# Kernel optimization log

Hardware: AMD Instinct MI355X
Metric: run time of the kernel (lower is better)

Reference implementation:

```python
import jax, jax.numpy as jnp
import numpy as np

DIM = 256
NUM_EXPERTS = 16
EXPERT_HIDDEN = 128
ROUTER_HIDDEN = 64
N_TOKENS = 32768


def setup_inputs() -> dict:
    key = jax.random.key(0)
    ks = jax.random.split(key, 9)
    s = lambda fan_in: 1.0 / np.sqrt(fan_in)
    x = jax.random.normal(ks[0], (N_TOKENS, DIM), dtype=jnp.float32)
    # Router params (Linear(DIM,64) -> ReLU -> Linear(64,E))
    r_w1 = jax.random.uniform(ks[1], (DIM, ROUTER_HIDDEN), jnp.float32, -s(DIM), s(DIM))
    r_b1 = jax.random.uniform(ks[2], (ROUTER_HIDDEN,), jnp.float32, -s(DIM), s(DIM))
    r_w2 = jax.random.uniform(ks[3], (ROUTER_HIDDEN, NUM_EXPERTS), jnp.float32, -s(ROUTER_HIDDEN), s(ROUTER_HIDDEN))
    r_b2 = jax.random.uniform(ks[4], (NUM_EXPERTS,), jnp.float32, -s(ROUTER_HIDDEN), s(ROUTER_HIDDEN))
    # Expert params, stacked over experts: Linear(DIM,128) -> Tanh -> Linear(128,DIM)
    e_w1 = jax.random.uniform(ks[5], (NUM_EXPERTS, DIM, EXPERT_HIDDEN), jnp.float32, -s(DIM), s(DIM))
    e_b1 = jax.random.uniform(ks[6], (NUM_EXPERTS, EXPERT_HIDDEN), jnp.float32, -s(DIM), s(DIM))
    e_w2 = jax.random.uniform(ks[7], (NUM_EXPERTS, EXPERT_HIDDEN, DIM), jnp.float32, -s(EXPERT_HIDDEN), s(EXPERT_HIDDEN))
    e_b2 = jax.random.uniform(ks[8], (NUM_EXPERTS, DIM), jnp.float32, -s(EXPERT_HIDDEN), s(EXPERT_HIDDEN))
    return {"x": x, "r_w1": r_w1, "r_b1": r_b1, "r_w2": r_w2, "r_b2": r_b2,
            "e_w1": e_w1, "e_b1": e_b1, "e_w2": e_w2, "e_b2": e_b2}


def reference(x, r_w1, r_b1, r_w2, r_b2, e_w1, e_b1, e_w2, e_b2):
    # Router: softmax(Linear(ReLU(Linear(x)))), temp=1.0
    h_r = jax.nn.relu(x @ r_w1 + r_b1)                      # [N, 64]
    w = jax.nn.softmax(h_r @ r_w2 + r_b2, axis=-1)          # [N, E]
    # All experts densely (faithful to the reference loop), batched over E.
    h = jnp.tanh(jnp.einsum('nd,edh->neh', x, e_w1) + e_b1[None, :, :])   # [N, E, H]
    outs = jnp.einsum('neh,ehd->ned', h, e_w2) + e_b2[None, :, :]         # [N, E, D]
    # Top-2 gating: mask, renormalize, combine.
    top_val, top_idx = jax.lax.top_k(w, 2)                  # [N, 2]
    n = w.shape[0]
    mask = jnp.zeros_like(w).at[jnp.arange(n)[:, None], top_idx].set(1.0)
    w_top = w * mask
    w_top = w_top / (jnp.sum(w_top, axis=-1, keepdims=True) + 1e-8)
    y_pred = jnp.einsum('ne,ned->nd', w_top, outs)          # [N, D]
    return (y_pred, w)
```

## Files before the change

kernel.cpp:

```cpp
#include <hip/hip_runtime.h>
#include <math.h>

#define NT 32768
#define DIM 256
#define NE 16
#define EH 128
#define RH 64
#define TB 64
#define NPERS 512

#define IB (NT * DIM)
#define WS_COUNTS (IB)
#define WS_OFFSETS (IB + 16)
#define WS_CURSORS (IB + 33)
#define WS_NBLK (IB + 49)
#define WS_TABLE (IB + 64)
#define WS_TOKE (IB + 4096)
#define WS_LIST (WS_TOKE + 2 * NT)
#define WS_TOKG (WS_LIST + 2 * NT)
#define WS_LIST_G (WS_TOKG + 2 * NT)
#define WS_END_I (WS_LIST_G + 2 * NT)
#define U_W1T (2 * WS_END_I)
#define U_W2T (U_W1T + NE * DIM * EH)
#define U_XG (U_W2T + NE * DIM * EH)

typedef __attribute__((ext_vector_type(4))) float f32x4;
typedef __attribute__((ext_vector_type(8))) short bf16x8;
typedef __attribute__((ext_vector_type(8))) unsigned short us8;

#define SWZ9(b) ((b) ^ (((b) >> 5) & 0x70))
#define SWZ8(b) ((b) ^ (((b) >> 4) & 0x70))

__device__ inline unsigned short f2bf(float f) {
    unsigned int bits = __builtin_bit_cast(unsigned int, f);
    bits += 0x7fffu + ((bits >> 16) & 1u);
    return (unsigned short)(bits >> 16);
}

__device__ inline float fast_tanh(float v) {
    float cv = fminf(fmaxf(v, -15.f), 15.f);
    float ex = __expf(2.f * cv);
    return (ex - 1.f) / (ex + 1.f);
}

__global__ __launch_bounds__(256) void router_kernel(
    const float* __restrict__ x,
    const float* __restrict__ rw1, const float* __restrict__ rb1,
    const float* __restrict__ rw2, const float* __restrict__ rb2,
    float* __restrict__ w_out, int* __restrict__ wsi, float* __restrict__ wsf)
{
    __shared__ float xT[64][68];
    __shared__ float w1s[64][64];
    __shared__ float hs[64][68];
    __shared__ float ls[64][20];
    __shared__ int scnt[16];

    const int tid = threadIdx.x;
    const int tok0 = blockIdx.x * 64;
    if (tid < 16) scnt[tid] = 0;

    float acc[4][4];
#pragma unroll
    for (int i = 0; i < 4; ++i)
#pragma unroll
        for (int j = 0; j < 4; ++j) acc[i][j] = 0.f;

    const int tt = (tid & 15) * 4;
    const int hh = (tid >> 4) * 4;

    for (int kc = 0; kc < 4; ++kc) {
        __syncthreads();
#pragma unroll
        for (int i = 0; i < 4; ++i) {
            int idx = tid + 256 * i;
            int t = idx >> 4;
            int d4 = (idx & 15) * 4;
            float4 v = *(const float4*)(x + (size_t)(tok0 + t) * DIM + kc * 64 + d4);
            xT[d4 + 0][t] = v.x; xT[d4 + 1][t] = v.y;
            xT[d4 + 2][t] = v.z; xT[d4 + 3][t] = v.w;
        }
#pragma unroll
        for (int i = 0; i < 4; ++i) {
            int idx = tid + 256 * i;
            int d = idx >> 4;
            int h4 = (idx & 15) * 4;
            *(float4*)&w1s[d][h4] = *(const float4*)(rw1 + (size_t)(kc * 64 + d) * RH + h4);
        }
        __syncthreads();
#pragma unroll 8
        for (int d = 0; d < 64; ++d) {
            const float4 xa4 = *(const float4*)&xT[d][tt];
            const float4 wv4 = *(const float4*)&w1s[d][hh];
            const float xa[4] = {xa4.x, xa4.y, xa4.z, xa4.w};
            const float wv[4] = {wv4.x, wv4.y, wv4.z, wv4.w};
#pragma unroll
            for (int i = 0; i < 4; ++i)
#pragma unroll
                for (int j = 0; j < 4; ++j)
                    acc[i][j] = fmaf(xa[i], wv[j], acc[i][j]);
        }
    }
    __syncthreads();
    {
        const float4 b4 = *(const float4*)(rb1 + hh);
        const float b[4] = {b4.x, b4.y, b4.z, b4.w};
#pragma unroll
        for (int i = 0; i < 4; ++i) {
            float4 hv;
            hv.x = fmaxf(acc[i][0] + b[0], 0.f);
            hv.y = fmaxf(acc[i][1] + b[1], 0.f);
            hv.z = fmaxf(acc[i][2] + b[2], 0.f);
            hv.w = fmaxf(acc[i][3] + b[3], 0.f);
            *(float4*)&hs[tt + i][hh] = hv;
        }
    }
    __syncthreads();
    {
        int tok = tid >> 2;
        int e0 = (tid & 3) * 4;
        float l[4] = {0.f, 0.f, 0.f, 0.f};
#pragma unroll 8
        for (int k = 0; k < 64; ++k) {
            float hv = hs[tok][k];
            float4 wv = *(const float4*)(rw2 + k * NE + e0);
            l[0] = fmaf(hv, wv.x, l[0]);
            l[1] = fmaf(hv, wv.y, l[1]);
            l[2] = fmaf(hv, wv.z, l[2]);
            l[3] = fmaf(hv, wv.w, l[3]);
        }
        float4 lb = *(const float4*)(rb2 + e0);
        ls[tok][e0 + 0] = l[0] + lb.x;
        ls[tok][e0 + 1] = l[1] + lb.y;
        ls[tok][e0 + 2] = l[2] + lb.z;
        ls[tok][e0 + 3] = l[3] + lb.w;
    }
    __syncthreads();
    if (tid < 64) {
        const int tok = tid;
        const int gt = tok0 + tok;
        float v[16];
        float m = -1e30f;
#pragma unroll
        for (int e = 0; e < 16; ++e) { v[e] = ls[tok][e]; m = fmaxf(m, v[e]); }
        float s = 0.f;
#pragma unroll
        for (int e = 0; e < 16; ++e) { v[e] = expf(v[e] - m); s += v[e]; }
        const float inv = 1.0f / s;
#pragma unroll
        for (int e = 0; e < 16; ++e) v[e] *= inv;
#pragma unroll
        for (int e = 0; e < 16; e += 4) {
            float4 wv = make_float4(v[e], v[e + 1], v[e + 2], v[e + 3]);
            *(float4*)(w_out + (size_t)gt * NE + e) = wv;
        }
        float v1 = -1.f, v2 = -1.f; int i1 = 0, i2 = 0;
#pragma unroll
        for (int e = 0; e < 16; ++e) {
            if (v[e] > v1) { v2 = v1; i2 = i1; v1 = v[e]; i1 = e; }
            else if (v[e] > v2) { v2 = v[e]; i2 = e; }
        }
        const float den = v1 + v2 + 1e-8f;
        atomicAdd(&scnt[i1], 1);
        atomicAdd(&scnt[i2], 1);
        wsi[WS_TOKE + 2 * gt + 0] = i1;
        wsi[WS_TOKE + 2 * gt + 1] = i2;
        wsf[WS_TOKG + 2 * gt + 0] = v1 / den;
        wsf[WS_TOKG + 2 * gt + 1] = v2 / den;
    }
    __syncthreads();
    if (tid < 16 && scnt[tid]) atomicAdd(&wsi[WS_COUNTS + tid], scnt[tid]);
}

__global__ __launch_bounds__(256) void wprep_kernel(
    const float* __restrict__ ew1, const float* __restrict__ ew2,
    unsigned short* __restrict__ w1t, unsigned short* __restrict__ w2t)
{
    __shared__ float t[64][65];
    int b = blockIdx.x;
    const float* src; unsigned short* dst; int R, C, tr, tc;
    if (b < 128) {
        int e = b >> 3, t8 = b & 7; tr = t8 >> 1; tc = t8 & 1;
        src = ew1 + (size_t)e * DIM * EH; R = DIM; C = EH;
        dst = w1t + (size_t)e * DIM * EH;
    } else {
        int b2 = b - 128; int e = b2 >> 3, t8 = b2 & 7; tr = t8 & 1; tc = t8 >> 1;
        src = ew2 + (size_t)e * EH * DIM; R = EH; C = DIM;
        dst = w2t + (size_t)e * EH * DIM;
    }
    const int R0 = tr * 64, C0 = tc * 64;
    const int tid = threadIdx.x;
#pragma unroll
    for (int q = 0; q < 4; ++q) {
        int r = (tid >> 4) + q * 16, c = (tid & 15) * 4;
        float4 v = *(const float4*)(src + (size_t)(R0 + r) * C + C0 + c);
        t[r][c] = v.x; t[r][c + 1] = v.y; t[r][c + 2] = v.z; t[r][c + 3] = v.w;
    }
    __syncthreads();
#pragma unroll
    for (int q = 0; q < 2; ++q) {
        int rp = (tid >> 3) + q * 32, c0 = (tid & 7) * 8;
        us8 u;
#pragma unroll
        for (int k = 0; k < 8; ++k) u[k] = f2bf(t[c0 + k][rp]);
        *(us8*)(dst + (size_t)(C0 + rp) * R + R0 + c0) = u;
    }
}

__global__ __launch_bounds__(64) void scan_kernel(int* __restrict__ wsi)
{
    __shared__ int soff[17], snc[16];
    const int tid = threadIdx.x;
    if (tid == 0) {
        int off = 0, nb = 0;
        soff[0] = 0;
        for (int e = 0; e < NE; ++e) {
            int c = wsi[WS_COUNTS + e];
            wsi[WS_CURSORS + e] = off;
            wsi[WS_OFFSETS + e] = off;
            off += c;
            soff[e + 1] = off;
            snc[e] = nb;
            nb += (c + TB - 1) / TB;
        }
        wsi[WS_OFFSETS + NE] = off;
        wsi[WS_NBLK] = nb;
    }
    __syncthreads();
    for (int e = 0; e < NE; ++e) {
        int nc = (soff[e + 1] - soff[e] + TB - 1) / TB;
        for (int k = tid; k < nc; k += 64)
            wsi[WS_TABLE + snc[e] + k] = (e << 16) | k;
    }
}

__global__ __launch_bounds__(256) void scatter_kernel(int* __restrict__ wsi, float* __restrict__ wsf)
{
    __shared__ int scnt[16], sbase[16];
    const int tid = threadIdx.x;
    const int t = blockIdx.x * 256 + tid;
    if (tid < 16) scnt[tid] = 0;
    __syncthreads();
    const int e0 = wsi[WS_TOKE + 2 * t + 0];
    const int e1 = wsi[WS_TOKE + 2 * t + 1];
    const int l0 = atomicAdd(&scnt[e0], 1);
    const int l1 = atomicAdd(&scnt[e1], 1);
    __syncthreads();
    if (tid < 16) sbase[tid] = scnt[tid] ? atomicAdd(&wsi[WS_CURSORS + tid], scnt[tid]) : 0;
    __syncthreads();
    const int p0 = sbase[e0] + l0;
    const int p1 = sbase[e1] + l1;
    wsi[WS_LIST + p0] = (t << 1);
    wsf[WS_LIST_G + p0] = wsf[WS_TOKG + 2 * t + 0];
    wsi[WS_LIST + p1] = (t << 1) | 1;
    wsf[WS_LIST_G + p1] = wsf[WS_TOKG + 2 * t + 1];
}

__global__ __launch_bounds__(256) void gather_kernel(
    const float* __restrict__ x, const int* __restrict__ wsi,
    unsigned short* __restrict__ xg)
{
    const int tid = threadIdx.x;
    const int p = blockIdx.x * 32 + (tid >> 3);
    const int sub = tid & 7;
    const int tok = wsi[WS_LIST + p] >> 1;
    const float* src = x + (size_t)tok * DIM + sub * 32;
    unsigned short* dst = xg + (size_t)p * DIM + sub * 32;
    float4 v[8];
#pragma unroll
    for (int i = 0; i < 8; ++i) v[i] = *(const float4*)(src + i * 4);
#pragma unroll
    for (int i = 0; i < 4; ++i) {
        us8 u;
        u[0] = f2bf(v[2 * i].x);     u[1] = f2bf(v[2 * i].y);
        u[2] = f2bf(v[2 * i].z);     u[3] = f2bf(v[2 * i].w);
        u[4] = f2bf(v[2 * i + 1].x); u[5] = f2bf(v[2 * i + 1].y);
        u[6] = f2bf(v[2 * i + 1].z); u[7] = f2bf(v[2 * i + 1].w);
        *(us8*)(dst + i * 8) = u;
    }
}

__global__ __launch_bounds__(256, 2) void expert_kernel(
    const unsigned short* __restrict__ xg,
    const float* __restrict__ eb1, const float* __restrict__ eb2,
    const unsigned short* __restrict__ w1t, const unsigned short* __restrict__ w2t,
    const int* __restrict__ wsi, const float* __restrict__ wsf,
    float* __restrict__ y, float* __restrict__ part1)
{
    __shared__ unsigned short smem[16384];
    __shared__ int sl[64];
    __shared__ float sg[64];

    const int nblk = wsi[WS_NBLK];
    const int tid = threadIdx.x;
    const int lane = tid & 63, w = tid >> 6;
    const int l15 = lane & 15;
    const int kq = lane >> 4;
    const int q4 = kq * 4;
    char* lds = (char*)smem;
    f32x4 zero4; zero4[0] = zero4[1] = zero4[2] = zero4[3] = 0.f;

    for (int bi = blockIdx.x; bi < nblk; bi += NPERS) {
        const int ent = wsi[WS_TABLE + bi];
        const int e = ent >> 16;
        const int c = ent & 0xffff;
        const int start = wsi[WS_OFFSETS + e] + c * TB;
        const int cnt = min(TB, wsi[WS_OFFSETS + e + 1] - start);

        __syncthreads();

        const char* xrow = (const char*)(xg + (size_t)start * DIM);
        us8 ubuf[8];
#pragma unroll
        for (int i = 0; i < 8; ++i)
            ubuf[i] = *(const us8*)(xrow + (tid + i * 256) * 16);

        const char* w1e = (const char*)(w1t + (size_t)e * DIM * EH);
        bf16x8 b1[8][2];
#pragma unroll
        for (int ks = 0; ks < 8; ++ks)
#pragma unroll
            for (int nt = 0; nt < 2; ++nt)
                b1[ks][nt] = *(const bf16x8*)(w1e + (w * 32 + nt * 16 + l15) * 512 + ks * 64 + kq * 16);

        if (tid < 64) {
            sl[tid] = (tid < cnt) ? wsi[WS_LIST + start + tid] : 0;
            sg[tid] = (tid < cnt) ? wsf[WS_LIST_G + start + tid] : 0.f;
        }

#pragma unroll
        for (int i = 0; i < 8; ++i)
            *(us8*)(lds + SWZ9((tid + i * 256) * 16)) = ubuf[i];
        __syncthreads();

        f32x4 acc[4][2];
#pragma unroll
        for (int i = 0; i < 4; ++i)
#pragma unroll
            for (int j = 0; j < 2; ++j) acc[i][j] = zero4;

#pragma unroll
        for (int ks = 0; ks < 8; ++ks) {
            bf16x8 a[4];
#pragma unroll
            for (int mt = 0; mt < 4; ++mt)
                a[mt] = *(const bf16x8*)(lds + SWZ9((mt * 16 + l15) * 512 + ks * 64 + kq * 16));
#pragma unroll
            for (int mt = 0; mt < 4; ++mt)
#pragma unroll
                for (int nt = 0; nt < 2; ++nt)
                    acc[mt][nt] = __builtin_amdgcn_mfma_f32_16x16x32_bf16(a[mt], b1[ks][nt], acc[mt][nt], 0, 0, 0);
        }

        const char* w2e = (const char*)(w2t + (size_t)e * EH * DIM);
        bf16x8 b2a[4][2];
#pragma unroll
        for (int ks = 0; ks < 4; ++ks)
#pragma unroll
            for (int nt = 0; nt < 2; ++nt)
                b2a[ks][nt] = *(const bf16x8*)(w2e + (w * 64 + nt * 16 + l15) * 256 + ks * 64 + kq * 16);

        __syncthreads();

#pragma unroll
        for (int nt = 0; nt < 2; ++nt) {
            const int h = w * 32 + nt * 16 + l15;
            const float b1v = eb1[e * EH + h];
#pragma unroll
            for (int mt = 0; mt < 4; ++mt)
#pragma unroll
                for (int r = 0; r < 4; ++r) {
                    int tok = mt * 16 + q4 + r;
                    *(unsigned short*)(lds + SWZ8(tok * 256 + h * 2)) = f2bf(fast_tanh(acc[mt][nt][r] + b1v));
                }
        }
        __syncthreads();

        bf16x8 b2b[4][2];
#pragma unroll
        for (int ks = 0; ks < 4; ++ks)
#pragma unroll
            for (int nt = 0; nt < 2; ++nt)
                b2b[ks][nt] = *(const bf16x8*)(w2e + (w * 64 + 32 + nt * 16 + l15) * 256 + ks * 64 + kq * 16);

        {
            f32x4 acc2[4][2];
#pragma unroll
            for (int i = 0; i < 4; ++i)
#pragma unroll
                for (int j = 0; j < 2; ++j) acc2[i][j] = zero4;
#pragma unroll
            for (int ks = 0; ks < 4; ++ks) {
                bf16x8 a[4];
#pragma unroll
                for (int mt = 0; mt < 4; ++mt)
                    a[mt] = *(const bf16x8*)(lds + SWZ8((mt * 16 + l15) * 256 + ks * 64 + kq * 16));
#pragma unroll
                for (int mt = 0; mt < 4; ++mt)
#pragma unroll
                    for (int nt = 0; nt < 2; ++nt)
                        acc2[mt][nt] = __builtin_amdgcn_mfma_f32_16x16x32_bf16(a[mt], b2a[ks][nt], acc2[mt][nt], 0, 0, 0);
            }
            float b2v[2];
#pragma unroll
            for (int nt = 0; nt < 2; ++nt)
                b2v[nt] = eb2[e * DIM + w * 64 + nt * 16 + l15];
#pragma unroll
            for (int mt = 0; mt < 4; ++mt)
#pragma unroll
                for (int r = 0; r < 4; ++r) {
                    int rl = mt * 16 + q4 + r;
                    if (rl < cnt) {
                        int entry = sl[rl];
                        float g = sg[rl];
                        float* dst = ((entry & 1) ? part1 : y) + (size_t)(entry >> 1) * DIM + w * 64;
#pragma unroll
                        for (int nt = 0; nt < 2; ++nt)
                            dst[nt * 16 + l15] = g * (acc2[mt][nt][r] + b2v[nt]);
                    }
                }
        }
        {
            f32x4 acc2[4][2];
#pragma unroll
            for (int i = 0; i < 4; ++i)
#pragma unroll
                for (int j = 0; j < 2; ++j) acc2[i][j] = zero4;
#pragma unroll
            for (int ks = 0; ks < 4; ++ks) {
                bf16x8 a[4];
#pragma unroll
                for (int mt = 0; mt < 4; ++mt)
                    a[mt] = *(const bf16x8*)(lds + SWZ8((mt * 16 + l15) * 256 + ks * 64 + kq * 16));
#pragma unroll
                for (int mt = 0; mt < 4; ++mt)
#pragma unroll
                    for (int nt = 0; nt < 2; ++nt)
                        acc2[mt][nt] = __builtin_amdgcn_mfma_f32_16x16x32_bf16(a[mt], b2b[ks][nt], acc2[mt][nt], 0, 0, 0);
            }
            float b2v[2];
#pragma unroll
            for (int nt = 0; nt < 2; ++nt)
                b2v[nt] = eb2[e * DIM + w * 64 + 32 + nt * 16 + l15];
#pragma unroll
            for (int mt = 0; mt < 4; ++mt)
#pragma unroll
                for (int r = 0; r < 4; ++r) {
                    int rl = mt * 16 + q4 + r;
                    if (rl < cnt) {
                        int entry = sl[rl];
                        float g = sg[rl];
                        float* dst = ((entry & 1) ? part1 : y) + (size_t)(entry >> 1) * DIM + w * 64 + 32;
#pragma unroll
                        for (int nt = 0; nt < 2; ++nt)
                            dst[nt * 16 + l15] = g * (acc2[mt][nt][r] + b2v[nt]);
                    }
                }
        }
    }
}

__global__ __launch_bounds__(256) void combine_kernel(float* __restrict__ y,
                                                      const float* __restrict__ part1)
{
    const size_t i = ((size_t)blockIdx.x * 256 + threadIdx.x) * 4;
    float4 a = *(float4*)(y + i);
    const float4 b = *(const float4*)(part1 + i);
    a.x += b.x; a.y += b.y; a.z += b.z; a.w += b.w;
    *(float4*)(y + i) = a;
}

extern "C" void kernel_launch(void* const* d_in, const int* in_sizes, int n_in,
                              void* d_out, int out_size, void* d_ws, size_t ws_size,
                              hipStream_t stream)
{
    const float* x = (const float*)d_in[0];
    const float* rw1 = (const float*)d_in[1];
    const float* rb1 = (const float*)d_in[2];
    const float* rw2 = (const float*)d_in[3];
    const float* rb2 = (const float*)d_in[4];
    const float* ew1 = (const float*)d_in[5];
    const float* eb1 = (const float*)d_in[6];
    const float* ew2 = (const float*)d_in[7];
    const float* eb2 = (const float*)d_in[8];

    float* y = (float*)d_out;
    float* w_out = y + (size_t)NT * DIM;
    int* wsi = (int*)d_ws;
    float* wsf = (float*)d_ws;
    float* part1 = (float*)d_ws;
    unsigned short* wsu = (unsigned short*)d_ws;

    hipMemsetAsync(wsi + WS_COUNTS, 0, NE * sizeof(int), stream);

    wprep_kernel<<<256, 256, 0, stream>>>(ew1, ew2, wsu + U_W1T, wsu + U_W2T);
    router_kernel<<<NT / 64, 256, 0, stream>>>(x, rw1, rb1, rw2, rb2, w_out, wsi, wsf);
    scan_kernel<<<1, 64, 0, stream>>>(wsi);
    scatter_kernel<<<NT / 256, 256, 0, stream>>>(wsi, wsf);
    gather_kernel<<<2 * NT / 32, 256, 0, stream>>>(x, wsi, wsu + U_XG);
    expert_kernel<<<NPERS, 256, 0, stream>>>(wsu + U_XG, eb1, eb2,
                                             wsu + U_W1T, wsu + U_W2T,
                                             wsi, wsf, y, part1);
    combine_kernel<<<NT * DIM / 1024, 256, 0, stream>>>(y, part1);
}
```

Baseline: 138.4 us.

## Stage expert outputs as contiguous bf16 rows and gather-combine with gates

The expert kernel now stages each tile's outputs in shared memory as bf16 and writes them as contiguous rows into a sorted linear buffer, instead of scattering fp32 rows gated into y and a part1 buffer. The scatter kernel records each token's inverse positions, and the combine kernel gathers the two bf16 rows per token, applies the gate weights and writes y once. This halves the intermediate output traffic, makes the expert stores coalesced, and removes the separate y read-modify-write. In exchange it adds bf16 rounding of expert outputs, a larger LDS footprint that may lower occupancy, and an extra barrier per tile.

```diff
diff --git a/kernel.cpp b/kernel.cpp
--- a/kernel.cpp
+++ b/kernel.cpp
@@ -18,8 +18,9 @@
 #define WS_TOKE (IB + 4096)
 #define WS_LIST (WS_TOKE + 2 * NT)
 #define WS_TOKG (WS_LIST + 2 * NT)
-#define WS_LIST_G (WS_TOKG + 2 * NT)
-#define WS_END_I (WS_LIST_G + 2 * NT)
+#define WS_INV (WS_TOKG + 2 * NT)
+#define WS_END_I (WS_INV + 2 * NT)
+#define U_OUT 0
 #define U_W1T (2 * WS_END_I)
 #define U_W2T (U_W1T + NE * DIM * EH)
 #define U_XG (U_W2T + NE * DIM * EH)
@@ -36,7 +37,10 @@
     bits += 0x7fffu + ((bits >> 16) & 1u);
     return (unsigned short)(bits >> 16);
 }
-
+__device__ inline float bf2f(unsigned short u) {
+    unsigned int v = ((unsigned int)u) << 16;
+    return __builtin_bit_cast(float, v);
+}
 __device__ inline float fast_tanh(float v) {
     float cv = fminf(fmaxf(v, -15.f), 15.f);
     float ex = __expf(2.f * cv);
@@ -233,7 +237,7 @@
     }
 }
 
-__global__ __launch_bounds__(256) void scatter_kernel(int* __restrict__ wsi, float* __restrict__ wsf)
+__global__ __launch_bounds__(256) void scatter_kernel(int* __restrict__ wsi)
 {
     __shared__ int scnt[16], sbase[16];
     const int tid = threadIdx.x;
@@ -249,10 +253,10 @@
     __syncthreads();
     const int p0 = sbase[e0] + l0;
     const int p1 = sbase[e1] + l1;
-    wsi[WS_LIST + p0] = (t << 1);
-    wsf[WS_LIST_G + p0] = wsf[WS_TOKG + 2 * t + 0];
-    wsi[WS_LIST + p1] = (t << 1) | 1;
-    wsf[WS_LIST_G + p1] = wsf[WS_TOKG + 2 * t + 1];
+    wsi[WS_LIST + p0] = t;
+    wsi[WS_LIST + p1] = t;
+    wsi[WS_INV + 2 * t + 0] = p0;
+    wsi[WS_INV + 2 * t + 1] = p1;
 }
 
 __global__ __launch_bounds__(256) void gather_kernel(
@@ -262,7 +266,7 @@
     const int tid = threadIdx.x;
     const int p = blockIdx.x * 32 + (tid >> 3);
     const int sub = tid & 7;
-    const int tok = wsi[WS_LIST + p] >> 1;
+    const int tok = wsi[WS_LIST + p];
     const float* src = x + (size_t)tok * DIM + sub * 32;
     unsigned short* dst = xg + (size_t)p * DIM + sub * 32;
     float4 v[8];
@@ -283,12 +287,11 @@
     const unsigned short* __restrict__ xg,
     const float* __restrict__ eb1, const float* __restrict__ eb2,
     const unsigned short* __restrict__ w1t, const unsigned short* __restrict__ w2t,
-    const int* __restrict__ wsi, const float* __restrict__ wsf,
-    float* __restrict__ y, float* __restrict__ part1)
+    const int* __restrict__ wsi,
+    unsigned short* __restrict__ out_lin)
 {
     __shared__ unsigned short smem[16384];
-    __shared__ int sl[64];
-    __shared__ float sg[64];
+    __shared__ unsigned short obufb[64 * 264];
 
     const int nblk = wsi[WS_NBLK];
     const int tid = threadIdx.x;
@@ -306,8 +309,6 @@
         const int start = wsi[WS_OFFSETS + e] + c * TB;
         const int cnt = min(TB, wsi[WS_OFFSETS + e + 1] - start);
 
-        __syncthreads();
-
         const char* xrow = (const char*)(xg + (size_t)start * DIM);
         us8 ubuf[8];
 #pragma unroll
@@ -321,11 +322,6 @@
 #pragma unroll
             for (int nt = 0; nt < 2; ++nt)
                 b1[ks][nt] = *(const bf16x8*)(w1e + (w * 32 + nt * 16 + l15) * 512 + ks * 64 + kq * 16);
-
-        if (tid < 64) {
-            sl[tid] = (tid < cnt) ? wsi[WS_LIST + start + tid] : 0;
-            sg[tid] = (tid < cnt) ? wsf[WS_LIST_G + start + tid] : 0.f;
-        }
 
 #pragma unroll
         for (int i = 0; i < 8; ++i)
@@ -407,17 +403,11 @@
 #pragma unroll
             for (int mt = 0; mt < 4; ++mt)
 #pragma unroll
-                for (int r = 0; r < 4; ++r) {
-                    int rl = mt * 16 + q4 + r;
-                    if (rl < cnt) {
-                        int entry = sl[rl];
-                        float g = sg[rl];
-                        float* dst = ((entry & 1) ? part1 : y) + (size_t)(entry >> 1) * DIM + w * 64;
-#pragma unroll
-                        for (int nt = 0; nt < 2; ++nt)
-                            dst[nt * 16 + l15] = g * (acc2[mt][nt][r] + b2v[nt]);
-                    }
-                }
+                for (int nt = 0; nt < 2; ++nt)
+#pragma unroll
+                    for (int r = 0; r < 4; ++r)
+                        obufb[(mt * 16 + q4 + r) * 264 + w * 64 + nt * 16 + l15] =
+                            f2bf(acc2[mt][nt][r] + b2v[nt]);
         }
         {
             f32x4 acc2[4][2];
@@ -444,29 +434,62 @@
 #pragma unroll
             for (int mt = 0; mt < 4; ++mt)
 #pragma unroll
-                for (int r = 0; r < 4; ++r) {
-                    int rl = mt * 16 + q4 + r;
-                    if (rl < cnt) {
-                        int entry = sl[rl];
-                        float g = sg[rl];
-                        float* dst = ((entry & 1) ? part1 : y) + (size_t)(entry >> 1) * DIM + w * 64 + 32;
-#pragma unroll
-                        for (int nt = 0; nt < 2; ++nt)
-                            dst[nt * 16 + l15] = g * (acc2[mt][nt][r] + b2v[nt]);
-                    }
-                }
-        }
-    }
-}
-
-__global__ __launch_bounds__(256) void combine_kernel(float* __restrict__ y,
-                                                      const float* __restrict__ part1)
-{
-    const size_t i = ((size_t)blockIdx.x * 256 + threadIdx.x) * 4;
-    float4 a = *(float4*)(y + i);
-    const float4 b = *(const float4*)(part1 + i);
-    a.x += b.x; a.y += b.y; a.z += b.z; a.w += b.w;
-    *(float4*)(y + i) = a;
+                for (int nt = 0; nt < 2; ++nt)
+#pragma unroll
+                    for (int r = 0; r < 4; ++r)
+                        obufb[(mt * 16 + q4 + r) * 264 + w * 64 + 32 + nt * 16 + l15] =
+                            f2bf(acc2[mt][nt][r] + b2v[nt]);
+        }
+        __syncthreads();
+
+        {
+            const int row = tid >> 2, sub = tid & 3;
+            if (row < cnt) {
+                const unsigned short* src = obufb + row * 264 + sub * 64;
+                unsigned short* dst = out_lin + (size_t)(start + row) * DIM + sub * 64;
+#pragma unroll
+                for (int i = 0; i < 8; ++i)
+                    *(us8*)(dst + i * 8) = *(const us8*)(src + i * 8);
+            }
+        }
+    }
+}
+
+__global__ __launch_bounds__(256) void combine_kernel(
+    const unsigned short* __restrict__ out_lin,
+    const int* __restrict__ wsi, const float* __restrict__ wsf,
+    float* __restrict__ y)
+{
+    const int tid = threadIdx.x;
+    const int t = blockIdx.x * 32 + (tid >> 3);
+    const int sub = tid & 7;
+    const int p0 = wsi[WS_INV + 2 * t + 0];
+    const int p1 = wsi[WS_INV + 2 * t + 1];
+    const float g0 = wsf[WS_TOKG + 2 * t + 0];
+    const float g1 = wsf[WS_TOKG + 2 * t + 1];
+    const unsigned short* a = out_lin + (size_t)p0 * DIM + sub * 32;
+    const unsigned short* b = out_lin + (size_t)p1 * DIM + sub * 32;
+    float* dst = y + (size_t)t * DIM + sub * 32;
+    us8 ua[4], ub[4];
+#pragma unroll
+    for (int i = 0; i < 4; ++i) {
+        ua[i] = *(const us8*)(a + i * 8);
+        ub[i] = *(const us8*)(b + i * 8);
+    }
+#pragma unroll
+    for (int i = 0; i < 4; ++i) {
+        float4 o0, o1;
+        o0.x = fmaf(g1, bf2f(ub[i][0]), g0 * bf2f(ua[i][0]));
+        o0.y = fmaf(g1, bf2f(ub[i][1]), g0 * bf2f(ua[i][1]));
+        o0.z = fmaf(g1, bf2f(ub[i][2]), g0 * bf2f(ua[i][2]));
+        o0.w = fmaf(g1, bf2f(ub[i][3]), g0 * bf2f(ua[i][3]));
+        o1.x = fmaf(g1, bf2f(ub[i][4]), g0 * bf2f(ua[i][4]));
+        o1.y = fmaf(g1, bf2f(ub[i][5]), g0 * bf2f(ua[i][5]));
+        o1.z = fmaf(g1, bf2f(ub[i][6]), g0 * bf2f(ua[i][6]));
+        o1.w = fmaf(g1, bf2f(ub[i][7]), g0 * bf2f(ua[i][7]));
+        *(float4*)(dst + i * 8) = o0;
+        *(float4*)(dst + i * 8 + 4) = o1;
+    }
 }
 
 extern "C" void kernel_launch(void* const* d_in, const int* in_sizes, int n_in,
@@ -487,7 +510,6 @@
     float* w_out = y + (size_t)NT * DIM;
     int* wsi = (int*)d_ws;
     float* wsf = (float*)d_ws;
-    float* part1 = (float*)d_ws;
     unsigned short* wsu = (unsigned short*)d_ws;
 
     hipMemsetAsync(wsi + WS_COUNTS, 0, NE * sizeof(int), stream);
@@ -495,10 +517,10 @@
     wprep_kernel<<<256, 256, 0, stream>>>(ew1, ew2, wsu + U_W1T, wsu + U_W2T);
     router_kernel<<<NT / 64, 256, 0, stream>>>(x, rw1, rb1, rw2, rb2, w_out, wsi, wsf);
     scan_kernel<<<1, 64, 0, stream>>>(wsi);
-    scatter_kernel<<<NT / 256, 256, 0, stream>>>(wsi, wsf);
+    scatter_kernel<<<NT / 256, 256, 0, stream>>>(wsi);
     gather_kernel<<<2 * NT / 32, 256, 0, stream>>>(x, wsi, wsu + U_XG);
     expert_kernel<<<NPERS, 256, 0, stream>>>(wsu + U_XG, eb1, eb2,
                                              wsu + U_W1T, wsu + U_W2T,
-                                             wsi, wsf, y, part1);
-    combine_kernel<<<NT * DIM / 1024, 256, 0, stream>>>(y, part1);
-}
+                                             wsi, wsu + U_OUT);
+    combine_kernel<<<NT / 32, 256, 0, stream>>>(wsu + U_OUT, wsi, wsf, y);
+}
```

Measured after the change: 121.3 us. 1.14x faster.
